# Kernel tuning notes

Hardware: AMD Instinct MI355X
Metric: run time of the kernel (lower is better)

Reference implementation:

```python
import jax, jax.numpy as jnp
import numpy as np

B, L, N = 8, 16, 256
P = 6.0
KSIZE = 5


def setup_inputs() -> dict:
    key = jax.random.key(0)
    k = jax.random.split(key, 7)
    return {
        "Z_re": jax.random.normal(k[0], (B, 1, N, N), dtype=jnp.float32),
        "Z_im": jax.random.normal(k[1], (B, 1, N, N), dtype=jnp.float32),
        "Masks_re": jax.random.normal(k[2], (L, N, N), dtype=jnp.float32),
        "Masks_im": jax.random.normal(k[3], (L, N, N), dtype=jnp.float32),
        "Ytr": jax.random.uniform(k[4], (B, L, N, N), dtype=jnp.float32),
        "W": jax.random.normal(k[5], (KSIZE, KSIZE, 1, 1), dtype=jnp.float32) * 0.05,
        "b": jnp.zeros((1,), dtype=jnp.float32),
    }


def _conv2d_same(x, W, b):
    # channels_first 'same' conv, 1 in / 1 out channel, kernel HWIO
    y = jax.lax.conv_general_dilated(
        x, W, window_strides=(1, 1), padding="SAME",
        dimension_numbers=("NCHW", "HWIO", "NCHW"))
    return y + b.reshape(1, 1, 1, 1)


def reference(Z_re, Z_im, Masks_re, Masks_im, Ytr, W, b):
    Z = jax.lax.complex(Z_re, Z_im)                      # (B,1,N,N)
    masks = jax.lax.complex(Masks_re, Masks_im)[None]     # (1,L,N,N)

    # A(Z) = fft2(masks * Z)  (CDP forward operator)
    AZ = jnp.fft.fft2(masks * Z)                          # (B,L,N,N)
    Y = Ytr.astype(AZ.dtype) * AZ                         # Ytr .* A(Z)
    # AT(Y) = sum_L conj(masks) * ifft2(Y)
    ATY = jnp.sum(jnp.conj(masks) * jnp.fft.ifft2(Y), axis=1, keepdims=True)  # (B,1,N,N)

    M = np.float32(N * N * L)
    R = np.float32(np.ceil(M / P))
    div = jnp.asarray(M * R, dtype=ATY.dtype)
    Znew = ATY / div

    # per-part learnable conv
    Zc = jax.lax.complex(_conv2d_same(Znew.real, W, b),
                         _conv2d_same(Znew.imag, W, b))

    # complex Frobenius norm over spatial axes, keepdims
    fro = jnp.sqrt(jnp.sum(Zc.real**2 + Zc.imag**2, axis=(2, 3), keepdims=True))
    Zc = Zc / fro.astype(Zc.dtype)
    # return real/imag stacked so output is a real array: (2,B,1,N,N)
    return jnp.stack([Zc.real, Zc.imag], axis=0)
```

## Files before the change

kernel.cpp:

```cpp
#include <hip/hip_runtime.h>
#include <hip/hip_fp16.h>
#include <math.h>

static constexpr int B_ = 8, L_ = 16, N_ = 256;
static constexpr int NN = N_ * N_;
static constexpr int IMGS = B_ * L_;

__device__ __forceinline__ float2 cmul(float2 a, float2 b) {
    return make_float2(a.x * b.x - a.y * b.y, a.x * b.y + a.y * b.x);
}

__device__ __forceinline__ void twinit(float2* tw, int tid) {
    float ang = -3.14159265358979323846f * (float)tid / 128.0f;
    float s, c;
    sincosf(ang, &s, &c);
    tw[tid] = make_float2(c, s);
}

template <bool INV>
__device__ __forceinline__ void dft4(const float2* x, float2* X) {
    float2 t0 = make_float2(x[0].x + x[2].x, x[0].y + x[2].y);
    float2 t1 = make_float2(x[0].x - x[2].x, x[0].y - x[2].y);
    float2 t2 = make_float2(x[1].x + x[3].x, x[1].y + x[3].y);
    float2 t3 = make_float2(x[1].x - x[3].x, x[1].y - x[3].y);
    X[0] = make_float2(t0.x + t2.x, t0.y + t2.y);
    X[2] = make_float2(t0.x - t2.x, t0.y - t2.y);
    if (!INV) {
        X[1] = make_float2(t1.x + t3.y, t1.y - t3.x);
        X[3] = make_float2(t1.x - t3.y, t1.y + t3.x);
    } else {
        X[1] = make_float2(t1.x - t3.y, t1.y + t3.x);
        X[3] = make_float2(t1.x + t3.y, t1.y - t3.x);
    }
}

template <bool INV>
__device__ __forceinline__ float2 w16mul(float2 v, int k) {
    constexpr float C = 0.92387953251128674f, S = 0.38268343236508978f,
                    R = 0.70710678118654746f;
    float re = 1.f, im = 0.f;
    switch (k) {
        case 0: return v;
        case 1: re = C;  im = -S; break;
        case 2: re = R;  im = -R; break;
        case 3: re = S;  im = -C; break;
        case 4: re = 0.f; im = -1.f; break;
        case 6: re = -R; im = -R; break;
        case 9: re = -C; im = S;  break;
    }
    if (INV) im = -im;
    return cmul(v, make_float2(re, im));
}

template <bool INV>
__device__ __forceinline__ void dft16(const float2* x, float2* y) {
    float2 A[4][4];
#pragma unroll
    for (int n0 = 0; n0 < 4; ++n0) {
        float2 in[4] = {x[n0], x[n0 + 4], x[n0 + 8], x[n0 + 12]};
        dft4<INV>(in, A[n0]);
    }
#pragma unroll
    for (int k1 = 0; k1 < 4; ++k1) {
#pragma unroll
        for (int n0 = 1; n0 < 4; ++n0) A[n0][k1] = w16mul<INV>(A[n0][k1], n0 * k1);
        float2 in[4] = {A[0][k1], A[1][k1], A[2][k1], A[3][k1]};
        float2 o[4];
        dft4<INV>(in, o);
#pragma unroll
        for (int k0 = 0; k0 < 4; ++k0) y[k1 + 4 * k0] = o[k0];
    }
}

template <bool INV>
__device__ __forceinline__ void fft256_r16(float2* r, float2* xg,
                                           const float2* tw, int a) {
    float2 y[16];
    dft16<INV>(r, y);
#pragma unroll
    for (int t = 1; t < 16; ++t) {
        float2 w = tw[a * t];
        if (INV) w.y = -w.y;
        y[t] = cmul(y[t], w);
    }
#pragma unroll
    for (int t = 0; t < 16; ++t) xg[t * 17 + a] = y[t];
    __syncthreads();
#pragma unroll
    for (int aa = 0; aa < 16; ++aa) r[aa] = xg[a * 17 + aa];
    dft16<INV>(r, y);
#pragma unroll
    for (int i = 0; i < 16; ++i) r[i] = y[i];
}

__global__ __launch_bounds__(256) void k_rowfft(
    const float* __restrict__ Zre, const float* __restrict__ Zim,
    const float* __restrict__ Mre, const float* __restrict__ Mim,
    __half2* __restrict__ T) {
    __shared__ float2 tw[256];
    __shared__ float2 xch[4368];
    int tid = threadIdx.x;
    twinit(tw, tid);
    __syncthreads();

    int g = tid >> 4, a = tid & 15;
    int rowg = blockIdx.x * 16 + g;
    int b = rowg >> 12, l = (rowg >> 8) & 15, row = rowg & 255;

    int zbase = (b << 16) + (row << 8);
    int mbase = (l << 16) + (row << 8);
    float2 r[16];
#pragma unroll
    for (int c = 0; c < 16; ++c) {
        int i = a + 16 * c;
        float2 z = make_float2(Zre[zbase + i], Zim[zbase + i]);
        float2 m = make_float2(Mre[mbase + i], Mim[mbase + i]);
        r[c] = cmul(m, z);
    }
    fft256_r16<false>(r, &xch[g * 273], tw, a);

    __half2* outp = T + (((size_t)(b * 16 + l)) << 16) + (row << 8);
#pragma unroll
    for (int d = 0; d < 16; ++d)
        outp[a + 16 * d] = __floats2half2_rn(r[d].x * 0.00390625f,
                                             r[d].y * 0.00390625f);
}

__global__ __launch_bounds__(256) void k_colpass(
    __half2* __restrict__ T, const float* __restrict__ Ytr) {
    __shared__ float2 tw[256];
    __shared__ float2 xch[4368];
    int tid = threadIdx.x;
    twinit(tw, tid);
    __syncthreads();

    int img = blockIdx.x >> 4;
    int c0 = (blockIdx.x & 15) << 4;
    int c = tid & 15, a = tid >> 4;
    size_t base = ((size_t)img << 16) + c0 + c;

    float2 r[16];
#pragma unroll
    for (int cc = 0; cc < 16; ++cc)
        r[cc] = __half22float2(T[base + ((a + 16 * cc) << 8)]);

    fft256_r16<false>(r, &xch[c * 273], tw, a);

#pragma unroll
    for (int d = 0; d < 16; ++d) {
        float y = Ytr[base + ((a + 16 * d) << 8)];
        r[d].x *= y;
        r[d].y *= y;
    }
    __syncthreads();

    fft256_r16<true>(r, &xch[c * 273], tw, a);

#pragma unroll
    for (int d = 0; d < 16; ++d)
        T[base + ((a + 16 * d) << 8)] = __floats2half2_rn(r[d].x, r[d].y);
}

__global__ __launch_bounds__(256) void k_rowifft_acc(
    const __half2* __restrict__ T,
    const float* __restrict__ Mre, const float* __restrict__ Mim,
    float2* __restrict__ P, float scale) {
    __shared__ float2 tw[256];
    __shared__ float2 xch[4368];
    int tid = threadIdx.x;
    twinit(tw, tid);
    __syncthreads();

    int g = tid >> 4, a = tid & 15;
    int rowg = blockIdx.x * 16 + g;
    int b = rowg >> 8, row = rowg & 255;
    int lg = blockIdx.y;

    float2 acc[16];
#pragma unroll
    for (int k = 0; k < 16; ++k) acc[k] = make_float2(0.f, 0.f);

#pragma unroll 1
    for (int li = 0; li < 4; ++li) {
        int l = (lg << 2) + li;
        const __half2* src = T + (((size_t)(b * 16 + l)) << 16) + (row << 8);
        float2 r[16];
#pragma unroll
        for (int c = 0; c < 16; ++c) r[c] = __half22float2(src[a + 16 * c]);
        __syncthreads();
        fft256_r16<true>(r, &xch[g * 273], tw, a);
        int mbase = (l << 16) + (row << 8);
#pragma unroll
        for (int d = 0; d < 16; ++d) {
            int i = a + 16 * d;
            float mr = Mre[mbase + i], mi = Mim[mbase + i];
            acc[d].x += mr * r[d].x + mi * r[d].y;
            acc[d].y += mr * r[d].y - mi * r[d].x;
        }
    }

    float2* dst = P + (((size_t)(lg * B_ + b)) << 16) + (row << 8);
#pragma unroll
    for (int d = 0; d < 16; ++d) {
        int i = a + 16 * d;
        dst[i] = make_float2(acc[d].x * scale, acc[d].y * scale);
    }
}

__global__ __launch_bounds__(256) void k_sum4(
    const float2* __restrict__ P, float2* __restrict__ ATY) {
    int i = blockIdx.x * 2048 + threadIdx.x;
#pragma unroll
    for (int k = 0; k < 8; ++k) {
        int p = i + (k << 8);
        float2 v0 = P[p];
        float2 v1 = P[p + (size_t)B_ * NN];
        float2 v2 = P[p + (size_t)2 * B_ * NN];
        float2 v3 = P[p + (size_t)3 * B_ * NN];
        ATY[p] = make_float2(v0.x + v1.x + v2.x + v3.x,
                             v0.y + v1.y + v2.y + v3.y);
    }
}

__global__ __launch_bounds__(256) void k_conv(
    const float2* __restrict__ ATY, const float* __restrict__ W,
    const float* __restrict__ bptr, float2* __restrict__ Zc,
    float* __restrict__ ssq_part) {
    __shared__ float wsh[25];
    __shared__ float red[256];
    int slice = blockIdx.x & 63;
    int b = blockIdx.x >> 6;
    int tid = threadIdx.x;
    if (tid < 25) wsh[tid] = W[tid];
    __syncthreads();
    float bias = bptr[0];

    const float2* img = ATY + ((size_t)b << 16);
    float2* zc = Zc + ((size_t)b << 16);
    int row0 = slice << 2;
    float ssq = 0.f;
#pragma unroll 1
    for (int k = 0; k < 4; ++k) {
        int h = row0 + k, w = tid;
        float ar = bias, ai = bias;
#pragma unroll
        for (int kh = 0; kh < 5; ++kh) {
            int hh = h + kh - 2;
            if (hh < 0 || hh > 255) continue;
#pragma unroll
            for (int kw = 0; kw < 5; ++kw) {
                int ww = w + kw - 2;
                if (ww < 0 || ww > 255) continue;
                float wgt = wsh[kh * 5 + kw];
                float2 v = img[(hh << 8) + ww];
                ar = fmaf(v.x, wgt, ar);
                ai = fmaf(v.y, wgt, ai);
            }
        }
        zc[(h << 8) + w] = make_float2(ar, ai);
        ssq = fmaf(ar, ar, fmaf(ai, ai, ssq));
    }
    red[tid] = ssq;
    __syncthreads();
#pragma unroll
    for (int off = 128; off > 0; off >>= 1) {
        if (tid < off) red[tid] += red[tid + off];
        __syncthreads();
    }
    if (tid == 0) ssq_part[blockIdx.x] = red[0];
}

__global__ __launch_bounds__(256) void k_norm(
    const float2* __restrict__ Zc, const float* __restrict__ ssq_part,
    float* __restrict__ out) {
    __shared__ float red[64];
    int slice = blockIdx.x & 15;
    int b = blockIdx.x >> 4;
    int tid = threadIdx.x;
    if (tid < 64) red[tid] = ssq_part[(b << 6) + tid];
    __syncthreads();
    if (tid < 16) red[tid] += red[tid + 16] + red[tid + 32] + red[tid + 48];
    __syncthreads();
    if (tid == 0) {
        float s = 0.f;
#pragma unroll
        for (int i = 0; i < 16; ++i) s += red[i];
        red[0] = s;
    }
    __syncthreads();
    float invf = 1.0f / sqrtf(red[0]);

    const float2* zc = Zc + ((size_t)b << 16);
    float* outRe = out + ((size_t)b << 16);
    float* outIm = out + ((size_t)(B_ + b) << 16);
#pragma unroll
    for (int k = 0; k < 16; ++k) {
        int pix = (slice << 12) + (k << 8) + tid;
        float2 v = zc[pix];
        outRe[pix] = v.x * invf;
        outIm[pix] = v.y * invf;
    }
}

extern "C" void kernel_launch(void* const* d_in, const int* in_sizes, int n_in,
                              void* d_out, int out_size, void* d_ws, size_t ws_size,
                              hipStream_t stream) {
    const float* Zre = (const float*)d_in[0];
    const float* Zim = (const float*)d_in[1];
    const float* Mre = (const float*)d_in[2];
    const float* Mim = (const float*)d_in[3];
    const float* Ytr = (const float*)d_in[4];
    const float* W   = (const float*)d_in[5];
    const float* bia = (const float*)d_in[6];
    float* out = (float*)d_out;

    __half2* T   = (__half2*)d_ws;
    float2*  P   = (float2*)(T + (size_t)IMGS * NN);
    float2*  ATY = P + (size_t)4 * B_ * NN;
    float2*  Zc  = ATY + (size_t)B_ * NN;
    float*   ssq = (float*)(Zc + (size_t)B_ * NN);

    const float scale = (float)(256.0 / (65536.0 * 1048576.0 * 174763.0));

    k_rowfft<<<dim3(IMGS * N_ / 16), dim3(256), 0, stream>>>(Zre, Zim, Mre, Mim, T);
    k_colpass<<<dim3(IMGS * 16), dim3(256), 0, stream>>>(T, Ytr);
    k_rowifft_acc<<<dim3(B_ * N_ / 16, 4), dim3(256), 0, stream>>>(T, Mre, Mim, P, scale);
    k_sum4<<<dim3(256), dim3(256), 0, stream>>>(P, ATY);
    k_conv<<<dim3(B_ * 64), dim3(256), 0, stream>>>(ATY, W, bia, Zc, ssq);
    k_norm<<<dim3(B_ * 16), dim3(256), 0, stream>>>(Zc, ssq, out);
}
```

Before: 172.3 us.

## Tile intermediate spectrum layout, split L into eight groups, store partials in half

The intermediate FFT buffer now uses a 16x16 tiled layout, so column-pass reads and writes touch contiguous 64-byte chunks instead of 1 KB-strided single elements. The row-iFFT accumulation splits the 16 masks into 8 groups instead of 4, doubling the grid for more parallelism. Partial sums are stored as half2 with a rescale, and a new 8-way reduction kernel sums them. This cuts memory traffic and strided access, at the cost of extra fp16 rounding on the partial sums and more partials to reduce.

```diff
diff --git a/kernel.cpp b/kernel.cpp
--- a/kernel.cpp
+++ b/kernel.cpp
@@ -5,9 +5,14 @@
 static constexpr int B_ = 8, L_ = 16, N_ = 256;
 static constexpr int NN = N_ * N_;
 static constexpr int IMGS = B_ * L_;
+static constexpr int LG = 8;
 
 __device__ __forceinline__ float2 cmul(float2 a, float2 b) {
     return make_float2(a.x * b.x - a.y * b.y, a.x * b.y + a.y * b.x);
+}
+
+__device__ __forceinline__ int tidx(int row, int col) {
+    return ((row >> 4) << 12) + ((col >> 4) << 8) + ((row & 15) << 4) + (col & 15);
 }
 
 __device__ __forceinline__ void twinit(float2* tw, int tid) {
@@ -119,11 +124,11 @@
     }
     fft256_r16<false>(r, &xch[g * 273], tw, a);
 
-    __half2* outp = T + (((size_t)(b * 16 + l)) << 16) + (row << 8);
+    __half2* outp = T + ((size_t)(b * 16 + l) << 16);
 #pragma unroll
     for (int d = 0; d < 16; ++d)
-        outp[a + 16 * d] = __floats2half2_rn(r[d].x * 0.00390625f,
-                                             r[d].y * 0.00390625f);
+        outp[tidx(row, a + 16 * d)] = __floats2half2_rn(r[d].x * 0.00390625f,
+                                                        r[d].y * 0.00390625f);
 }
 
 __global__ __launch_bounds__(256) void k_colpass(
@@ -137,18 +142,19 @@
     int img = blockIdx.x >> 4;
     int c0 = (blockIdx.x & 15) << 4;
     int c = tid & 15, a = tid >> 4;
-    size_t base = ((size_t)img << 16) + c0 + c;
+    size_t ibase = (size_t)img << 16;
+    int colg = c0 + c;
 
     float2 r[16];
 #pragma unroll
     for (int cc = 0; cc < 16; ++cc)
-        r[cc] = __half22float2(T[base + ((a + 16 * cc) << 8)]);
+        r[cc] = __half22float2(T[ibase + tidx(a + 16 * cc, colg)]);
 
     fft256_r16<false>(r, &xch[c * 273], tw, a);
 
 #pragma unroll
     for (int d = 0; d < 16; ++d) {
-        float y = Ytr[base + ((a + 16 * d) << 8)];
+        float y = Ytr[ibase + ((a + 16 * d) << 8) + colg];
         r[d].x *= y;
         r[d].y *= y;
     }
@@ -158,13 +164,13 @@
 
 #pragma unroll
     for (int d = 0; d < 16; ++d)
-        T[base + ((a + 16 * d) << 8)] = __floats2half2_rn(r[d].x, r[d].y);
+        T[ibase + tidx(a + 16 * d, colg)] = __floats2half2_rn(r[d].x, r[d].y);
 }
 
 __global__ __launch_bounds__(256) void k_rowifft_acc(
     const __half2* __restrict__ T,
     const float* __restrict__ Mre, const float* __restrict__ Mim,
-    float2* __restrict__ P, float scale) {
+    __half2* __restrict__ P) {
     __shared__ float2 tw[256];
     __shared__ float2 xch[4368];
     int tid = threadIdx.x;
@@ -181,12 +187,13 @@
     for (int k = 0; k < 16; ++k) acc[k] = make_float2(0.f, 0.f);
 
 #pragma unroll 1
-    for (int li = 0; li < 4; ++li) {
-        int l = (lg << 2) + li;
-        const __half2* src = T + (((size_t)(b * 16 + l)) << 16) + (row << 8);
+    for (int li = 0; li < 16 / LG; ++li) {
+        int l = lg * (16 / LG) + li;
+        const __half2* src = T + ((size_t)(b * 16 + l) << 16);
         float2 r[16];
 #pragma unroll
-        for (int c = 0; c < 16; ++c) r[c] = __half22float2(src[a + 16 * c]);
+        for (int c = 0; c < 16; ++c)
+            r[c] = __half22float2(src[tidx(row, a + 16 * c)]);
         __syncthreads();
         fft256_r16<true>(r, &xch[g * 273], tw, a);
         int mbase = (l << 16) + (row << 8);
@@ -199,26 +206,29 @@
         }
     }
 
-    float2* dst = P + (((size_t)(lg * B_ + b)) << 16) + (row << 8);
+    const float s1 = 0.000244140625f;
+    __half2* dst = P + (((size_t)(lg * B_ + b)) << 16) + (row << 8);
 #pragma unroll
     for (int d = 0; d < 16; ++d) {
         int i = a + 16 * d;
-        dst[i] = make_float2(acc[d].x * scale, acc[d].y * scale);
-    }
-}
-
-__global__ __launch_bounds__(256) void k_sum4(
-    const float2* __restrict__ P, float2* __restrict__ ATY) {
+        dst[i] = __floats2half2_rn(acc[d].x * s1, acc[d].y * s1);
+    }
+}
+
+__global__ __launch_bounds__(256) void k_sum8(
+    const __half2* __restrict__ P, float2* __restrict__ ATY, float s2) {
     int i = blockIdx.x * 2048 + threadIdx.x;
 #pragma unroll
     for (int k = 0; k < 8; ++k) {
         int p = i + (k << 8);
-        float2 v0 = P[p];
-        float2 v1 = P[p + (size_t)B_ * NN];
-        float2 v2 = P[p + (size_t)2 * B_ * NN];
-        float2 v3 = P[p + (size_t)3 * B_ * NN];
-        ATY[p] = make_float2(v0.x + v1.x + v2.x + v3.x,
-                             v0.y + v1.y + v2.y + v3.y);
+        float sx = 0.f, sy = 0.f;
+#pragma unroll
+        for (int lg = 0; lg < LG; ++lg) {
+            float2 v = __half22float2(P[p + (size_t)lg * B_ * NN]);
+            sx += v.x;
+            sy += v.y;
+        }
+        ATY[p] = make_float2(sx * s2, sy * s2);
     }
 }
 
@@ -315,17 +325,17 @@
     float* out = (float*)d_out;
 
     __half2* T   = (__half2*)d_ws;
-    float2*  P   = (float2*)(T + (size_t)IMGS * NN);
-    float2*  ATY = P + (size_t)4 * B_ * NN;
+    __half2* P   = T + (size_t)IMGS * NN;
+    float2*  ATY = (float2*)(P + (size_t)LG * B_ * NN);
     float2*  Zc  = ATY + (size_t)B_ * NN;
     float*   ssq = (float*)(Zc + (size_t)B_ * NN);
 
-    const float scale = (float)(256.0 / (65536.0 * 1048576.0 * 174763.0));
+    const float s2 = (float)(1.0 / (65536.0 * 174763.0));
 
     k_rowfft<<<dim3(IMGS * N_ / 16), dim3(256), 0, stream>>>(Zre, Zim, Mre, Mim, T);
     k_colpass<<<dim3(IMGS * 16), dim3(256), 0, stream>>>(T, Ytr);
-    k_rowifft_acc<<<dim3(B_ * N_ / 16, 4), dim3(256), 0, stream>>>(T, Mre, Mim, P, scale);
-    k_sum4<<<dim3(256), dim3(256), 0, stream>>>(P, ATY);
+    k_rowifft_acc<<<dim3(B_ * N_ / 16, LG), dim3(256), 0, stream>>>(T, Mre, Mim, P);
+    k_sum8<<<dim3(256), dim3(256), 0, stream>>>(P, ATY, s2);
     k_conv<<<dim3(B_ * 64), dim3(256), 0, stream>>>(ATY, W, bia, Zc, ssq);
     k_norm<<<dim3(B_ * 16), dim3(256), 0, stream>>>(Zc, ssq, out);
 }
```

Measured after the change: 157.5 us. 8.6% less time.
